# Optimization experiments

Measured on AMD Instinct MI355X. Metric: run time of the kernel, lower is better.

## Reference

```python
import jax, jax.numpy as jnp
import numpy as np

N_NODES_PER_GRAPH = 64
NUM_GRAPHS = 2048
N = NUM_GRAPHS * N_NODES_PER_GRAPH  # 131072 total nodes
E = N * 8                           # 1048576 edges
IN_DIM, H1, H2 = 64, 128, 64
OUT_DIM = (N_NODES_PER_GRAPH * N_NODES_PER_GRAPH - N_NODES_PER_GRAPH) // 2  # 2016


def setup_inputs() -> dict:
    key = jax.random.key(0)
    ks = jax.random.split(key, 16)
    s = 0.05
    x = jax.random.normal(ks[0], (N, IN_DIM), dtype=jnp.float32)
    # edges within each graph: offsets within graph + graph base offset
    src_local = jax.random.randint(ks[1], (E,), 0, N_NODES_PER_GRAPH)
    dst_local = jax.random.randint(ks[2], (E,), 0, N_NODES_PER_GRAPH)
    gid = jnp.repeat(jnp.arange(NUM_GRAPHS), E // NUM_GRAPHS) * N_NODES_PER_GRAPH
    edge_index = jnp.stack([src_local + gid, dst_local + gid]).astype(jnp.int64)
    batch = jnp.repeat(jnp.arange(NUM_GRAPHS), N_NODES_PER_GRAPH).astype(jnp.int64)
    eps = jax.random.normal(ks[3], (NUM_GRAPHS, H2), dtype=jnp.float32)
    return {
        "x": x, "edge_index": edge_index, "batch": batch, "eps": eps,
        "w1_rel": jax.random.normal(ks[4], (IN_DIM, H1)) * s,
        "b1": jnp.zeros((H1,), jnp.float32),
        "w1_root": jax.random.normal(ks[5], (IN_DIM, H1)) * s,
        "w2_rel": jax.random.normal(ks[6], (H1, H2)) * s,
        "b2": jnp.zeros((H2,), jnp.float32),
        "w2_root": jax.random.normal(ks[7], (H1, H2)) * s,
        "w3_rel": jax.random.normal(ks[8], (H1, H2)) * s,
        "b3": jnp.zeros((H2,), jnp.float32),
        "w3_root": jax.random.normal(ks[9], (H1, H2)) * s,
        "fc1_w": jax.random.normal(ks[10], (H2, H1)) * s,
        "fc1_b": jnp.zeros((H1,), jnp.float32),
        "fc2_w": jax.random.normal(ks[11], (H1, OUT_DIM)) * s,
        "fc2_b": jnp.zeros((OUT_DIM,), jnp.float32),
    }


def _graph_conv(h, src, dst, w_rel, b, w_root):
    # PyG GraphConv: out_i = W_rel @ (sum_{j in N(i)} h_j) + b + W_root @ h_i
    agg = jax.ops.segment_sum(h[src], dst, num_segments=N)  # [N, d_in]
    return agg @ w_rel + b + h @ w_root


def _segment_mean(h, seg):
    s = jax.ops.segment_sum(h, seg, num_segments=NUM_GRAPHS)
    cnt = jax.ops.segment_sum(jnp.ones((h.shape[0],), h.dtype), seg, num_segments=NUM_GRAPHS)
    return s / jnp.maximum(cnt, 1.0)[:, None]


def reference(x, edge_index, batch, eps, w1_rel, b1, w1_root, w2_rel, b2, w2_root,
              w3_rel, b3, w3_root, fc1_w, fc1_b, fc2_w, fc2_b):
    src, dst = edge_index[0], edge_index[1]
    # encode (dropout p=0.0 -> identity)
    h1 = jax.nn.relu(_graph_conv(x, src, dst, w1_rel, b1, w1_root))
    mu = _segment_mean(_graph_conv(h1, src, dst, w2_rel, b2, w2_root), batch)
    logvar = _segment_mean(_graph_conv(h1, src, dst, w3_rel, b3, w3_root), batch)
    # reparameterize with provided eps
    z = mu + eps * jnp.exp(0.5 * logvar)
    # decode
    h = jax.nn.relu(z @ fc1_w + fc1_b)
    recon = jax.nn.sigmoid(h @ fc2_w + fc2_b)
    return recon, mu, logvar
```

## Files before the change

kernel.cpp:

```cpp
#include <hip/hip_runtime.h>
#include <math.h>

#define NG 2048
#define NPG 64
#define EPG 512
#define ETOT (NG*EPG)
#define IND 64
#define H1D 128
#define H2D 64
#define OUTD 2016

typedef __attribute__((ext_vector_type(8))) short bf16x8;
typedef __attribute__((ext_vector_type(4))) float f32x4;

__device__ inline short f2b(float f) {
  union { float f; unsigned u; } v; v.f = f;
  unsigned r = (v.u + 0x7FFFu + ((v.u >> 16) & 1u)) >> 16;
  return (short)r;
}

__global__ void p_w1(const float* __restrict__ w1_rel, const float* __restrict__ w1_root,
                     short* __restrict__ WTgF) {
  const int ct = blockIdx.x;
  const int ks = threadIdx.x >> 6, l = threadIdx.x & 63;
  const int col = ct*16 + (l & 15);
  const int kb  = ks*32 + (l >> 4)*8;
  short tmp[8];
  #pragma unroll
  for (int j = 0; j < 8; ++j) {
    const int k = kb + j;
    float v = (k < 64) ? w1_rel[k*H1D + col] : w1_root[(k - 64)*H1D + col];
    tmp[j] = f2b(v);
  }
  *(uint4*)&WTgF[(size_t)((ct*4 + ks)*64 + l)*8] = *(uint4*)tmp;
}

__global__ __launch_bounds__(256, 4) void k1_encoder(
    const float* __restrict__ x, const int* __restrict__ ei,
    const short* __restrict__ WTgF, const float* __restrict__ b1,
    short* __restrict__ SVg,
    const float* __restrict__ fc2_w, const float* __restrict__ w2_rel, const float* __restrict__ w2_root,
    const float* __restrict__ w3_rel, const float* __restrict__ w3_root,
    const float* __restrict__ fc1_w,
    short* __restrict__ WF2g, short* __restrict__ W23T, short* __restrict__ fc1T)
{
  __shared__ __align__(16) char smem[33792];
  const int g = blockIdx.x;
  const int tid = threadIdx.x;

  if (g >= NG) {
    float* L = (float*)smem;
    const int bid = g - NG;
    if (bid < 63) {
      const int c0 = bid*32;
      for (int i = tid; i < 4096; i += 256) {
        int k = i >> 5, c = i & 31;
        L[k*33 + c] = fc2_w[(size_t)k*OUTD + c0 + c];
      }
      __syncthreads();
      const int tl = tid >> 7;
      const int r  = tid & 127;
      const int ks = r >> 5;
      const int lp = r & 31;
      const int ct = bid*2 + tl;
      #pragma unroll
      for (int u = 0; u < 2; ++u) {
        const int l = lp*2 + u;
        const int cl = tl*16 + (l & 15);
        const int kb = ks*32 + (l >> 4)*8;
        short tmp[8];
        #pragma unroll
        for (int j = 0; j < 8; ++j) tmp[j] = f2b(L[(kb + j)*33 + cl]);
        *(uint4*)&WF2g[(size_t)((ct*4 + ks)*64 + l)*8] = *(uint4*)tmp;
      }
    } else if (bid < 67) {
      const int cc = bid - 63;
      const int j0 = cc*32;
      const float* wrel  = (cc < 2) ? w2_rel  : w3_rel;
      const float* wroot = (cc < 2) ? w2_root : w3_root;
      const int jl = j0 & 63;
      for (int i = tid; i < 4096; i += 256) {
        int k = i >> 5, c = i & 31;
        L[k*33 + c]        = wrel [k*H2D + jl + c];
        L[4224 + k*33 + c] = wroot[k*H2D + jl + c];
      }
      __syncthreads();
      const int c = tid >> 3, k0 = (tid & 7)*32;
      for (int kk = 0; kk < 32; ++kk) {
        int k = k0 + kk;
        float v = (k < 128) ? L[k*33 + c] : L[4224 + (k - 128)*33 + c];
        W23T[(size_t)(j0 + c)*264 + k] = f2b(v);
      }
    } else {
      const int c0 = (bid - 67)*64;
      for (int i = tid; i < 4096; i += 256) {
        int k = i >> 6, c = i & 63;
        L[k*65 + c] = fc1_w[k*H1D + c0 + c];
      }
      __syncthreads();
      const int c = tid >> 2, k0 = (tid & 3)*16;
      for (int kk = 0; kk < 16; ++kk)
        fc1T[(size_t)(c0 + c)*72 + k0 + kk] = f2b(L[(k0 + kk)*65 + c]);
    }
    return;
  }

  short* Xb   = (short*)smem;
  short* XbT  = (short*)(smem + 9216);
  short* Ab   = (short*)(smem + 18432);
  unsigned* Au32 = (unsigned*)(smem + 27648);
  float* deg  = (float*)(smem + 32000);
  float* hsum = (float*)(smem + 32256);
  float* wsum = (float*)(smem + 32768);

  const int w = tid >> 6, l = tid & 63;

  const int e0 = g*EPG + tid*2;
  const int s0 = ei[e0] & 63,     d0 = ei[ETOT + e0] & 63;
  const int s1 = ei[e0 + 1] & 63, d1 = ei[ETOT + e0 + 1] & 63;

  for (int i = tid; i < 64*17; i += 256) Au32[i] = 0u;
  if (tid < 128) { hsum[tid] = 0.f; wsum[tid] = 0.f; }

  {
    const int n = tid >> 2, f0 = (tid & 3) * 16;
    const float* xr = x + (size_t)g*(NPG*IND) + n*IND + f0;
    float4 v0 = *(const float4*)&xr[0];
    float4 v1 = *(const float4*)&xr[4];
    float4 v2 = *(const float4*)&xr[8];
    float4 v3 = *(const float4*)&xr[12];
    short b[16];
    b[0]=f2b(v0.x); b[1]=f2b(v0.y); b[2]=f2b(v0.z); b[3]=f2b(v0.w);
    b[4]=f2b(v1.x); b[5]=f2b(v1.y); b[6]=f2b(v1.z); b[7]=f2b(v1.w);
    b[8]=f2b(v2.x); b[9]=f2b(v2.y); b[10]=f2b(v2.z); b[11]=f2b(v2.w);
    b[12]=f2b(v3.x); b[13]=f2b(v3.y); b[14]=f2b(v3.z); b[15]=f2b(v3.w);
    short* xbp = &Xb[n*72 + f0];
    #pragma unroll
    for (int j = 0; j < 16; ++j) xbp[j] = b[j];
    #pragma unroll
    for (int j = 0; j < 16; ++j) XbT[(f0 + j)*72 + n] = b[j];
  }
  __syncthreads();

  atomicAdd(&Au32[d0*17 + (s0 >> 2)], 1u << (8*(s0 & 3)));
  atomicAdd(&Au32[d1*17 + (s1 >> 2)], 1u << (8*(s1 & 3)));
  __syncthreads();

  {
    const int row = tid >> 2, qw = tid & 3;
    unsigned wds[4];
    #pragma unroll
    for (int q = 0; q < 4; ++q) wds[q] = Au32[row*17 + qw*4 + q];
    unsigned* abp = (unsigned*)&Ab[row*72 + qw*16];
    #pragma unroll
    for (int q = 0; q < 4; ++q) {
      unsigned wv = wds[q];
      #pragma unroll
      for (int p = 0; p < 2; ++p) {
        unsigned c0 = (wv >> (16*p)) & 255u, c1 = (wv >> (16*p + 8)) & 255u;
        abp[q*2 + p] = (unsigned)(unsigned short)f2b((float)c0)
                     | ((unsigned)(unsigned short)f2b((float)c1) << 16);
      }
    }
  }
  if (tid < 16) {
    unsigned s = 0;
    #pragma unroll 8
    for (int d = 0; d < 64; ++d) s += Au32[d*17 + tid];
    deg[tid*4 + 0] = (float)(s & 255u);
    deg[tid*4 + 1] = (float)((s >> 8) & 255u);
    deg[tid*4 + 2] = (float)((s >> 16) & 255u);
    deg[tid*4 + 3] = (float)(s >> 24);
  }

  const int rm = w*16;
  const int fr = l & 15;
  const int koff = (l >> 4) * 8;

  f32x4 agc[4];
  #pragma unroll
  for (int t = 0; t < 4; ++t) agc[t] = (f32x4){0.f,0.f,0.f,0.f};
  #pragma unroll
  for (int ks = 0; ks < 2; ++ks) {
    bf16x8 a = *(const bf16x8*)&Ab[(rm + fr)*72 + ks*32 + koff];
    #pragma unroll
    for (int t = 0; t < 4; ++t) {
      bf16x8 b = *(const bf16x8*)&XbT[(t*16 + fr)*72 + ks*32 + koff];
      agc[t] = __builtin_amdgcn_mfma_f32_16x16x32_bf16(a, b, agc[t], 0, 0, 0);
    }
  }
  short* AGb = Ab;
  #pragma unroll
  for (int t = 0; t < 4; ++t)
    #pragma unroll
    for (int r = 0; r < 4; ++r)
      AGb[(rm + (l>>4)*4 + r)*72 + t*16 + fr] = f2b(agc[t][r]);
  __syncthreads();

  {
    float dg[4];
    #pragma unroll
    for (int r = 0; r < 4; ++r) dg[r] = deg[rm + (l>>4)*4 + r];

    bf16x8 afr[4];
    #pragma unroll
    for (int ks = 0; ks < 4; ++ks)
      afr[ks] = (ks < 2)
        ? *(const bf16x8*)&AGb[(rm + fr)*72 + ks*32 + koff]
        : *(const bf16x8*)&Xb[(rm + fr)*72 + (ks-2)*32 + koff];

    f32x4 acc[8];
    #pragma unroll
    for (int t = 0; t < 8; ++t) acc[t] = (f32x4){0.f,0.f,0.f,0.f};
    #pragma unroll
    for (int t = 0; t < 8; ++t)
      #pragma unroll
      for (int ks = 0; ks < 4; ++ks) {
        bf16x8 b = *(const bf16x8*)&WTgF[(size_t)((t*4 + ks)*64 + l)*8];
        acc[t] = __builtin_amdgcn_mfma_f32_16x16x32_bf16(afr[ks], b, acc[t], 0, 0, 0);
      }

    #pragma unroll
    for (int t = 0; t < 8; ++t) {
      const int col = t*16 + fr;
      const float bb = b1[col];
      float hs = 0.f, ws = 0.f;
      #pragma unroll
      for (int r = 0; r < 4; ++r) {
        float v = fmaxf(acc[t][r] + bb, 0.f);
        hs += v; ws += dg[r]*v;
      }
      hs += __shfl_down(hs, 32); ws += __shfl_down(ws, 32);
      hs += __shfl_down(hs, 16); ws += __shfl_down(ws, 16);
      if (l < 16) { atomicAdd(&hsum[col], hs); atomicAdd(&wsum[col], ws); }
    }
  }
  __syncthreads();

  if (tid < 128) {
    SVg[(size_t)g*256 + tid]       = f2b(wsum[tid]);
    SVg[(size_t)g*256 + 128 + tid] = f2b(hsum[tid]);
  }
}

__global__ __launch_bounds__(256) void k1b_latent(
    const short* __restrict__ SVg, const short* __restrict__ W23T,
    const float* __restrict__ b2, const float* __restrict__ b3,
    const float* __restrict__ eps, const short* __restrict__ fc1T,
    const float* __restrict__ fc1_b,
    float* __restrict__ out_mu, float* __restrict__ out_lv, short* __restrict__ hbufB)
{
  __shared__ short SV[32*264];
  __shared__ short Zt[32*72];
  const int g0 = blockIdx.x * 32;
  const int tid = threadIdx.x;
  const int w = tid >> 6, l = tid & 63;
  const int s = w >> 1;
  const int h = w & 1;
  const int fr = l & 15;
  const int koff = (l >> 4) * 8;

  {
    const uint4* src = (const uint4*)(SVg + (size_t)g0*256);
    for (int i = tid; i < 1024; i += 256) {
      int r = i >> 5, k0 = (i & 31) * 8;
      *(uint4*)&SV[r*264 + k0] = src[i];
    }
  }
  __syncthreads();

  f32x4 acc[4];
  #pragma unroll
  for (int t = 0; t < 4; ++t) acc[t] = (f32x4){0.f,0.f,0.f,0.f};
  #pragma unroll
  for (int ks = 0; ks < 8; ++ks) {
    bf16x8 a = *(const bf16x8*)&SV[(s*16 + fr)*264 + ks*32 + koff];
    #pragma unroll
    for (int j = 0; j < 2; ++j) {
      bf16x8 bm = *(const bf16x8*)&W23T[((2*h + j)*16 + fr)*264 + ks*32 + koff];
      bf16x8 bl = *(const bf16x8*)&W23T[((2*h + j + 4)*16 + fr)*264 + ks*32 + koff];
      acc[j]     = __builtin_amdgcn_mfma_f32_16x16x32_bf16(a, bm, acc[j], 0, 0, 0);
      acc[2 + j] = __builtin_amdgcn_mfma_f32_16x16x32_bf16(a, bl, acc[2 + j], 0, 0, 0);
    }
  }
  #pragma unroll
  for (int j = 0; j < 2; ++j) {
    const int col = (2*h + j)*16 + fr;
    const float bb2 = b2[col], bb3 = b3[col];
    #pragma unroll
    for (int r = 0; r < 4; ++r) {
      const int row = s*16 + (l>>4)*4 + r;
      const size_t gg = (size_t)(g0 + row);
      float mu = acc[j][r]     * (1.f/64.f) + bb2;
      float lv = acc[2 + j][r] * (1.f/64.f) + bb3;
      out_mu[gg*64 + col] = mu;
      out_lv[gg*64 + col] = lv;
      float z = mu + eps[gg*64 + col] * __expf(0.5f*lv);
      Zt[row*72 + col] = f2b(z);
    }
  }
  __syncthreads();

  f32x4 hacc[4];
  #pragma unroll
  for (int t = 0; t < 4; ++t) hacc[t] = (f32x4){0.f,0.f,0.f,0.f};
  #pragma unroll
  for (int ks = 0; ks < 2; ++ks) {
    bf16x8 a = *(const bf16x8*)&Zt[(s*16 + fr)*72 + ks*32 + koff];
    #pragma unroll
    for (int j = 0; j < 4; ++j) {
      bf16x8 b = *(const bf16x8*)&fc1T[((h*4 + j)*16 + fr)*72 + ks*32 + koff];
      hacc[j] = __builtin_amdgcn_mfma_f32_16x16x32_bf16(a, b, hacc[j], 0, 0, 0);
    }
  }
  #pragma unroll
  for (int j = 0; j < 4; ++j) {
    const int col = (h*4 + j)*16 + fr;
    const float bb = fc1_b[col];
    #pragma unroll
    for (int r = 0; r < 4; ++r) {
      const int row = s*16 + (l>>4)*4 + r;
      hbufB[(size_t)(g0 + row)*H1D + col] = f2b(fmaxf(hacc[j][r] + bb, 0.f));
    }
  }
}

__global__ __launch_bounds__(256, 4) void k2_decoder(
    const short* __restrict__ hbufB, const short* __restrict__ WF2g,
    const float* __restrict__ fc2_b, float* __restrict__ recon)
{
  __shared__ __align__(16) short Hb[64*136];
  const int bx = blockIdx.x, by = blockIdx.y;
  const int tid = threadIdx.x;
  const int w = tid >> 6, l = tid & 63;

  {
    const uint4* src = (const uint4*)(hbufB + (size_t)bx*64*H1D);
    for (int i = tid; i < 1024; i += 256) {
      int r = i >> 4, k0 = (i & 15) * 8;
      *(uint4*)&Hb[r*136 + k0] = src[i];
    }
  }
  __syncthreads();

  const int fr = l & 15;
  const int koff = (l >> 4) * 8;

  f32x4 acc[6];
  #pragma unroll
  for (int t = 0; t < 6; ++t) acc[t] = (f32x4){0.f,0.f,0.f,0.f};

  #pragma unroll
  for (int ks = 0; ks < 4; ++ks) {
    bf16x8 a = *(const bf16x8*)&Hb[(w*16 + fr)*136 + ks*32 + koff];
    #pragma unroll
    for (int t = 0; t < 6; ++t) {
      const int ct = by*6 + t;
      bf16x8 b = *(const bf16x8*)&WF2g[(size_t)((ct*4 + ks)*64 + l)*8];
      acc[t] = __builtin_amdgcn_mfma_f32_16x16x32_bf16(a, b, acc[t], 0, 0, 0);
    }
  }

  #pragma unroll
  for (int t = 0; t < 6; ++t) {
    const int col = by*96 + t*16 + fr;
    const float bb = fc2_b[col];
    #pragma unroll
    for (int r = 0; r < 4; ++r) {
      const int row = bx*64 + w*16 + (l>>4)*4 + r;
      float v = acc[t][r] + bb;
      recon[(size_t)row*OUTD + col] = 1.f/(1.f + __expf(-v));
    }
  }
}

extern "C" void kernel_launch(void* const* d_in, const int* in_sizes, int n_in,
                              void* d_out, int out_size, void* d_ws, size_t ws_size,
                              hipStream_t stream) {
  const float* x       = (const float*)d_in[0];
  const int*   ei      = (const int*)d_in[1];
  const float* eps     = (const float*)d_in[3];
  const float* w1_rel  = (const float*)d_in[4];
  const float* b1      = (const float*)d_in[5];
  const float* w1_root = (const float*)d_in[6];
  const float* w2_rel  = (const float*)d_in[7];
  const float* b2      = (const float*)d_in[8];
  const float* w2_root = (const float*)d_in[9];
  const float* w3_rel  = (const float*)d_in[10];
  const float* b3      = (const float*)d_in[11];
  const float* w3_root = (const float*)d_in[12];
  const float* fc1_w   = (const float*)d_in[13];
  const float* fc1_b   = (const float*)d_in[14];
  const float* fc2_w   = (const float*)d_in[15];
  const float* fc2_b   = (const float*)d_in[16];

  float* recon  = (float*)d_out;
  float* out_mu = recon + (size_t)NG*OUTD;
  float* out_lv = out_mu + (size_t)NG*H2D;

  char* p = (char*)d_ws;
  short* WTgF  = (short*)p;              p += 8*4*64*8*2;
  short* WF2g  = (short*)p;              p += 126*4*64*8*2;
  short* fc1T  = (short*)p;              p += 128*72*2;
  short* W23T  = (short*)p;              p += 128*264*2;
  short* SVg   = (short*)p;              p += (size_t)NG*256*2;
  short* hbufB = (short*)p;

  p_w1<<<8, 256, 0, stream>>>(w1_rel, w1_root, WTgF);
  k1_encoder<<<NG + 69, 256, 0, stream>>>(x, ei, WTgF, b1, SVg,
      fc2_w, w2_rel, w2_root, w3_rel, w3_root, fc1_w, WF2g, W23T, fc1T);
  k1b_latent<<<64, 256, 0, stream>>>(SVg, W23T, b2, b3, eps, fc1T, fc1_b,
                                     out_mu, out_lv, hbufB);
  k2_decoder<<<dim3(32, 21), 256, 0, stream>>>(hbufB, WF2g, fc2_b, recon);
}
```

Baseline: 154.3 us.

## Shrink encoder shared memory to 32KB and raise occupancy to 5 blocks

Measured after the change: 152.1 us. About the same (-1.4%).

```diff
diff --git a/kernel.cpp b/kernel.cpp
--- a/kernel.cpp
+++ b/kernel.cpp
@@ -35,7 +35,7 @@
   *(uint4*)&WTgF[(size_t)((ct*4 + ks)*64 + l)*8] = *(uint4*)tmp;
 }
 
-__global__ __launch_bounds__(256, 4) void k1_encoder(
+__global__ __launch_bounds__(256, 5) void k1_encoder(
     const float* __restrict__ x, const int* __restrict__ ei,
     const short* __restrict__ WTgF, const float* __restrict__ b1,
     short* __restrict__ SVg,
@@ -44,7 +44,7 @@
     const float* __restrict__ fc1_w,
     short* __restrict__ WF2g, short* __restrict__ W23T, short* __restrict__ fc1T)
 {
-  __shared__ __align__(16) char smem[33792];
+  __shared__ __align__(16) char smem[32768];
   const int g = blockIdx.x;
   const int tid = threadIdx.x;
 
@@ -79,18 +79,24 @@
       const float* wrel  = (cc < 2) ? w2_rel  : w3_rel;
       const float* wroot = (cc < 2) ? w2_root : w3_root;
       const int jl = j0 & 63;
+      const int c = tid >> 3, k0 = (tid & 7)*32;
       for (int i = tid; i < 4096; i += 256) {
-        int k = i >> 5, c = i & 31;
-        L[k*33 + c]        = wrel [k*H2D + jl + c];
-        L[4224 + k*33 + c] = wroot[k*H2D + jl + c];
+        int k = i >> 5, cc2 = i & 31;
+        L[k*33 + cc2] = wrel[k*H2D + jl + cc2];
       }
       __syncthreads();
-      const int c = tid >> 3, k0 = (tid & 7)*32;
-      for (int kk = 0; kk < 32; ++kk) {
-        int k = k0 + kk;
-        float v = (k < 128) ? L[k*33 + c] : L[4224 + (k - 128)*33 + c];
-        W23T[(size_t)(j0 + c)*264 + k] = f2b(v);
-      }
+      if (k0 < 128)
+        for (int kk = 0; kk < 32; ++kk)
+          W23T[(size_t)(j0 + c)*264 + k0 + kk] = f2b(L[(k0 + kk)*33 + c]);
+      __syncthreads();
+      for (int i = tid; i < 4096; i += 256) {
+        int k = i >> 5, cc2 = i & 31;
+        L[k*33 + cc2] = wroot[k*H2D + jl + cc2];
+      }
+      __syncthreads();
+      if (k0 >= 128)
+        for (int kk = 0; kk < 32; ++kk)
+          W23T[(size_t)(j0 + c)*264 + k0 + kk] = f2b(L[(k0 + kk - 128)*33 + c]);
     } else {
       const int c0 = (bid - 67)*64;
       for (int i = tid; i < 4096; i += 256) {
@@ -109,9 +115,8 @@
   short* XbT  = (short*)(smem + 9216);
   short* Ab   = (short*)(smem + 18432);
   unsigned* Au32 = (unsigned*)(smem + 27648);
-  float* deg  = (float*)(smem + 32000);
-  float* hsum = (float*)(smem + 32256);
-  float* wsum = (float*)(smem + 32768);
+  float* hsum = (float*)(smem + 31744);
+  float* wsum = (float*)(smem + 32256);
 
   const int w = tid >> 6, l = tid & 63;
 
@@ -119,7 +124,7 @@
   const int s0 = ei[e0] & 63,     d0 = ei[ETOT + e0] & 63;
   const int s1 = ei[e0 + 1] & 63, d1 = ei[ETOT + e0 + 1] & 63;
 
-  for (int i = tid; i < 64*17; i += 256) Au32[i] = 0u;
+  for (int i = tid; i < 64*16; i += 256) Au32[i] = 0u;
   if (tid < 128) { hsum[tid] = 0.f; wsum[tid] = 0.f; }
 
   {
@@ -142,15 +147,15 @@
   }
   __syncthreads();
 
-  atomicAdd(&Au32[d0*17 + (s0 >> 2)], 1u << (8*(s0 & 3)));
-  atomicAdd(&Au32[d1*17 + (s1 >> 2)], 1u << (8*(s1 & 3)));
+  atomicAdd(&Au32[d0*16 + (s0 >> 2)], 1u << (8*(s0 & 3)));
+  atomicAdd(&Au32[d1*16 + (s1 >> 2)], 1u << (8*(s1 & 3)));
   __syncthreads();
 
   {
     const int row = tid >> 2, qw = tid & 3;
     unsigned wds[4];
     #pragma unroll
-    for (int q = 0; q < 4; ++q) wds[q] = Au32[row*17 + qw*4 + q];
+    for (int q = 0; q < 4; ++q) wds[q] = Au32[row*16 + qw*4 + q];
     unsigned* abp = (unsigned*)&Ab[row*72 + qw*16];
     #pragma unroll
     for (int q = 0; q < 4; ++q) {
@@ -163,14 +168,21 @@
       }
     }
   }
-  if (tid < 16) {
-    unsigned s = 0;
-    #pragma unroll 8
-    for (int d = 0; d < 64; ++d) s += Au32[d*17 + tid];
-    deg[tid*4 + 0] = (float)(s & 255u);
-    deg[tid*4 + 1] = (float)((s >> 8) & 255u);
-    deg[tid*4 + 2] = (float)((s >> 16) & 255u);
-    deg[tid*4 + 3] = (float)(s >> 24);
+
+  float dg[4];
+  {
+    unsigned ps = 0;
+    #pragma unroll
+    for (int i = 0; i < 4; ++i) ps += Au32[((l >> 2) + 16*i)*16 + 4*w + (l & 3)];
+    ps += __shfl_xor(ps, 4);
+    ps += __shfl_xor(ps, 8);
+    ps += __shfl_xor(ps, 16);
+    ps += __shfl_xor(ps, 32);
+    unsigned dword = __shfl(ps, (l >> 4));
+    dg[0] = (float)(dword & 255u);
+    dg[1] = (float)((dword >> 8) & 255u);
+    dg[2] = (float)((dword >> 16) & 255u);
+    dg[3] = (float)(dword >> 24);
   }
 
   const int rm = w*16;
@@ -198,10 +210,6 @@
   __syncthreads();
 
   {
-    float dg[4];
-    #pragma unroll
-    for (int r = 0; r < 4; ++r) dg[r] = deg[rm + (l>>4)*4 + r];
-
     bf16x8 afr[4];
     #pragma unroll
     for (int ks = 0; ks < 4; ++ks)
```
